# Kernel optimization log

Hardware: AMD Instinct MI355X
Metric: run time of the kernel (lower is better)

## Reference

```python
import jax, jax.numpy as jnp
import numpy as np

WINDOW_SIZE = 20
NEG_BIG = -1e8  # matches -10**8 in the torch mask


def band_mask(S):
    # 0 inside the sliding window |i-j| <= WINDOW_SIZE, -1e8 outside (additive mask)
    idx = jnp.arange(S)
    return jnp.where(jnp.abs(idx[:, None] - idx[None, :]) <= WINDOW_SIZE, 0.0, NEG_BIG).astype(jnp.float32)


def setup_inputs() -> dict:
    key = jax.random.key(0)
    k1, k2, k3, k4 = jax.random.split(key, 4)
    B, S, Dq, Dk = 8, 2048, 1024, 1024
    queries = jax.random.normal(k1, (B, S, Dq), dtype=jnp.float32)
    keys = jax.random.normal(k2, (B, S, Dk), dtype=jnp.float32)
    # reduce = nn.Linear(key_dim, query_dim) since key_dim >= query_dim
    lim = 1.0 / np.sqrt(Dk)
    W_reduce = jax.random.uniform(k3, (Dq, Dk), jnp.float32, -lim, lim)
    b_reduce = jax.random.uniform(k4, (Dq,), jnp.float32, -lim, lim)
    return {"queries": queries, "keys": keys, "W_reduce": W_reduce, "b_reduce": b_reduce}


def reference(queries, keys, W_reduce, b_reduce):
    # values default to the ORIGINAL keys (before dim matching)
    values = keys
    # match_dims: reduce keys to query_dim
    keys_r = jnp.einsum('bkd,qd->bkq', keys, W_reduce) + b_reduce  # [B,S,Dq]
    sims = jnp.einsum('bqd,bkd->bqk', queries, keys_r)             # [B,S,S]
    sims = sims + band_mask(queries.shape[1])                      # additive banded window mask
    weights = jax.nn.softmax(sims, axis=-1)
    return jnp.einsum('bqk,bkd->bqd', weights, values)
```

## Files before the change

kernel.cpp:

```cpp
#include <hip/hip_runtime.h>


#define BATCH 8
#define SEQ   2048
#define DIM   1024
#define WIN   20

typedef _Float16 half8  __attribute__((ext_vector_type(8)));
typedef _Float16 half4v __attribute__((ext_vector_type(4)));
typedef float    f32x4  __attribute__((ext_vector_type(4)));

#define GLOAD_LDS16(gsrc, ldst)                                                        \
    __builtin_amdgcn_global_load_lds(                                                  \
        (const __attribute__((address_space(1))) void*)(gsrc),                         \
        (__attribute__((address_space(3))) void*)(ldst), 16, 0, 0)

__global__ __launch_bounds__(256) void cvt_q_f16(const float* __restrict__ in,
                                                 _Float16* __restrict__ out) {
    const int n8 = (BATCH * SEQ * DIM) / 8;
    for (int i = blockIdx.x * 256 + threadIdx.x; i < n8; i += gridDim.x * 256) {
        const float4 a = ((const float4*)in)[2 * i];
        const float4 b = ((const float4*)in)[2 * i + 1];
        half8 h;
        h[0] = (_Float16)a.x; h[1] = (_Float16)a.y; h[2] = (_Float16)a.z; h[3] = (_Float16)a.w;
        h[4] = (_Float16)b.x; h[5] = (_Float16)b.y; h[6] = (_Float16)b.z; h[7] = (_Float16)b.w;
        ((half8*)out)[i] = h;
    }
}

#define WTS 68
__global__ __launch_bounds__(256) void cvt_w_t(const float* __restrict__ W,
                                               _Float16* __restrict__ WT) {
    __shared__ _Float16 tile[64 * WTS];
    const int k0 = blockIdx.x * 64;
    const int n0 = blockIdx.y * 64;
    const int t  = threadIdx.x;
    const int r  = t >> 4;
    const int c4 = (t & 15) * 4;
    #pragma unroll
    for (int rr = 0; rr < 64; rr += 16) {
        float4 v = *(const float4*)&W[(size_t)(k0 + rr + r) * DIM + n0 + c4];
        _Float16* dst = &tile[(rr + r) * WTS + c4];
        dst[0] = (_Float16)v.x; dst[1] = (_Float16)v.y;
        dst[2] = (_Float16)v.z; dst[3] = (_Float16)v.w;
    }
    __syncthreads();
    #pragma unroll
    for (int rr = 0; rr < 64; rr += 16) {
        const int n = rr + r;
        half4v h = { tile[(c4 + 0) * WTS + n], tile[(c4 + 1) * WTS + n],
                     tile[(c4 + 2) * WTS + n], tile[(c4 + 3) * WTS + n] };
        *(half4v*)&WT[(size_t)(n0 + n) * DIM + k0 + c4] = h;
    }
}

#define GK 64
__global__ __launch_bounds__(256, 2) void gemm_f16t(const _Float16* __restrict__ A,
                                                    const _Float16* __restrict__ B,
                                                    _Float16* __restrict__ C) {
    __shared__ _Float16 As[128 * GK];
    __shared__ _Float16 Bs[128 * GK];

    const int m0   = blockIdx.y * 128;
    const int n0   = blockIdx.x * 128;
    const int t    = threadIdx.x;
    const int lane = t & 63;
    const int wv   = t >> 6;
    const int wm   = (wv >> 1) * 64;
    const int wn   = (wv & 1) * 64;
    const int l15  = lane & 15;
    const int quad = lane >> 4;

    const int srow = lane >> 3;
    const int sck  = (lane & 7) ^ srow;

    f32x4 acc[4][4] = {};

    for (int k0 = 0; k0 < DIM; k0 += GK) {
        __syncthreads();
        #pragma unroll
        for (int j = 0; j < 4; ++j) {
            const int rs = (j * 4 + wv) * 8;
            GLOAD_LDS16(A + (size_t)(m0 + rs + srow) * DIM + k0 + sck * 8, &As[rs * GK]);
            GLOAD_LDS16(B + (size_t)(n0 + rs + srow) * DIM + k0 + sck * 8, &Bs[rs * GK]);
        }
        __syncthreads();

        #pragma unroll
        for (int s = 0; s < 2; ++s) {
            half8 af[4], bf[4];
            #pragma unroll
            for (int i = 0; i < 4; ++i)
                af[i] = *(const half8*)&As[(wm + i * 16 + l15) * GK +
                                           (((s * 4 + quad) ^ (l15 & 7)) * 8)];
            #pragma unroll
            for (int j = 0; j < 4; ++j)
                bf[j] = *(const half8*)&Bs[(wn + j * 16 + l15) * GK +
                                           (((s * 4 + quad) ^ (l15 & 7)) * 8)];
            #pragma unroll
            for (int i = 0; i < 4; ++i)
                #pragma unroll
                for (int j = 0; j < 4; ++j)
                    acc[i][j] = __builtin_amdgcn_mfma_f32_16x16x32_f16(af[i], bf[j], acc[i][j], 0, 0, 0);
        }
    }

    #pragma unroll
    for (int i = 0; i < 4; ++i) {
        #pragma unroll
        for (int r = 0; r < 4; ++r) {
            _Float16* crow = C + (size_t)(m0 + wm + i * 16 + quad * 4 + r) * DIM + n0 + wn + l15;
            #pragma unroll
            for (int j = 0; j < 4; ++j)
                crow[j * 16] = (_Float16)acc[i][j][r];
        }
    }
}

#define TQV  32
#define KSR  96
#define KLD2 80
#define QLD2 80
#define SLD2 84
#define PLD  104

__global__ __launch_bounds__(512, 4) void attn_v5(const _Float16* __restrict__ QT,
                                                  const float* __restrict__ Keys,
                                                  float* __restrict__ Out) {
    const int blk  = blockIdx.x;
    const int b    = blk & 7;
    const int tile = blk >> 3;
    const int q0   = tile * TQV;
    const int t    = threadIdx.x;
    const int lane = t & 63;
    const int wv   = t >> 6;
    const int l15  = lane & 15;
    const int quad = lane >> 4;

    const int klo = (q0 - WIN) > 0 ? (q0 - WIN) : 0;
    const int khi = (q0 + TQV - 1 + WIN) < (SEQ - 1) ? (q0 + TQV - 1 + WIN) : (SEQ - 1);
    const int nk  = khi - klo + 1;

    const float* keys = Keys + (size_t)b * SEQ * DIM;

    __shared__ _Float16 Qc[TQV * QLD2];
    __shared__ _Float16 Ks[KSR * KLD2];
    __shared__ float    Sl[TQV * SLD2];
    __shared__ _Float16 Pl[TQV * PLD];

    const int qr = t >> 4;
    const int qc = (t & 15) * 4;
    const int kr = t >> 3;
    const int kc = (t & 7) * 8;
    const int krow0 = (klo + kr) < (SEQ - 1) ? (klo + kr) : (SEQ - 1);
    const int kr2   = 64 + (t >> 3);
    const int krow2 = (klo + kr2) < (SEQ - 1) ? (klo + kr2) : (SEQ - 1);

    const _Float16* qsrc  = QT + ((size_t)b * SEQ + q0 + qr) * DIM + qc;
    const float*    ksrc0 = keys + (size_t)krow0 * DIM + kc;
    const float*    ksrc2 = keys + (size_t)krow2 * DIM + kc;

    const int qt_w = wv >> 2;
    const int kt_a = wv & 3;
    const bool two = (kt_a == 0);

    f32x4 acc0 = {}, acc1 = {};

    for (int d0 = 0; d0 < DIM; d0 += 64) {
        half4v hq = *(const half4v*)(qsrc + d0);
        float4 kv0 = *(const float4*)(ksrc0 + d0);
        float4 kv1 = *(const float4*)(ksrc0 + d0 + 4);
        float4 kv2, kv3;
        if (t < 128) {
            kv2 = *(const float4*)(ksrc2 + d0);
            kv3 = *(const float4*)(ksrc2 + d0 + 4);
        }

        __syncthreads();

        *(half4v*)&Qc[qr * QLD2 + qc] = hq;
        half8 h0;
        h0[0] = (_Float16)kv0.x; h0[1] = (_Float16)kv0.y;
        h0[2] = (_Float16)kv0.z; h0[3] = (_Float16)kv0.w;
        h0[4] = (_Float16)kv1.x; h0[5] = (_Float16)kv1.y;
        h0[6] = (_Float16)kv1.z; h0[7] = (_Float16)kv1.w;
        *(half8*)&Ks[kr * KLD2 + kc] = h0;
        if (t < 128) {
            half8 h2;
            h2[0] = (_Float16)kv2.x; h2[1] = (_Float16)kv2.y;
            h2[2] = (_Float16)kv2.z; h2[3] = (_Float16)kv2.w;
            h2[4] = (_Float16)kv3.x; h2[5] = (_Float16)kv3.y;
            h2[6] = (_Float16)kv3.z; h2[7] = (_Float16)kv3.w;
            *(half8*)&Ks[kr2 * KLD2 + kc] = h2;
        }

        __syncthreads();

        #pragma unroll
        for (int s = 0; s < 2; ++s) {
            half8 af = *(const half8*)&Qc[(qt_w * 16 + l15) * QLD2 + s * 32 + quad * 8];
            half8 bf0 = *(const half8*)&Ks[(kt_a * 16 + l15) * KLD2 + s * 32 + quad * 8];
            acc0 = __builtin_amdgcn_mfma_f32_16x16x32_f16(af, bf0, acc0, 0, 0, 0);
            if (two) {
                half8 bf1 = *(const half8*)&Ks[(4 * 16 + l15) * KLD2 + s * 32 + quad * 8];
                acc1 = __builtin_amdgcn_mfma_f32_16x16x32_f16(af, bf1, acc1, 0, 0, 0);
            }
        }
    }

    __syncthreads();
    #pragma unroll
    for (int r = 0; r < 4; ++r) {
        const int q = qt_w * 16 + quad * 4 + r;
        {
            const int c = kt_a * 16 + l15;
            const int d = (q0 + q) - (klo + c);
            const bool valid = (c < nk) && ((unsigned)(d + WIN) <= 2u * WIN);
            Sl[q * SLD2 + c] = valid ? acc0[r] : -1e30f;
        }
        if (two) {
            const int c = 64 + l15;
            const int d = (q0 + q) - (klo + c);
            const bool valid = (c < nk) && ((unsigned)(d + WIN) <= 2u * WIN);
            Sl[q * SLD2 + c] = valid ? acc1[r] : -1e30f;
        }
    }
    __syncthreads();

    if (t < 128) {
        const int q = t >> 2, part = t & 3;
        const float* srow = &Sl[q * SLD2 + part * 20];
        _Float16*    prow = &Pl[q * PLD + part * 20];
        float m = -1e30f;
        float e[20];
        #pragma unroll
        for (int i = 0; i < 20; ++i) m = fmaxf(m, srow[i]);
        m = fmaxf(m, __shfl_xor(m, 1));
        m = fmaxf(m, __shfl_xor(m, 2));
        float ssum = 0.f;
        #pragma unroll
        for (int i = 0; i < 20; ++i) { e[i] = expf(srow[i] - m); ssum += e[i]; }
        ssum += __shfl_xor(ssum, 1);
        ssum += __shfl_xor(ssum, 2);
        const float inv = 1.f / ssum;
        #pragma unroll
        for (int i = 0; i < 20; ++i) prow[i] = (_Float16)(e[i] * inv);
        if (part == 3) {
            #pragma unroll
            for (int i = 0; i < 16; ++i) Pl[q * PLD + 80 + i] = (_Float16)0.f;
        }
    }
    __syncthreads();

    const int dt_w = wv & 3;
    const int kr2b  = 64 + (t >> 3);
    const int krow2b = (klo + kr2b) < (SEQ - 1) ? (klo + kr2b) : (SEQ - 1);
    const float* ksrc2b = keys + (size_t)krow2b * DIM + kc;

    for (int ch = 0; ch < 16; ++ch) {
        const int d0 = ch * 64;
        float4 kv0 = *(const float4*)(ksrc0 + d0);
        float4 kv1 = *(const float4*)(ksrc0 + d0 + 4);
        float4 kv2, kv3;
        if (t < 256) {
            kv2 = *(const float4*)(ksrc2b + d0);
            kv3 = *(const float4*)(ksrc2b + d0 + 4);
        }

        __syncthreads();

        half8 h0;
        h0[0] = (_Float16)kv0.x; h0[1] = (_Float16)kv0.y;
        h0[2] = (_Float16)kv0.z; h0[3] = (_Float16)kv0.w;
        h0[4] = (_Float16)kv1.x; h0[5] = (_Float16)kv1.y;
        h0[6] = (_Float16)kv1.z; h0[7] = (_Float16)kv1.w;
        *(half8*)&Ks[kr * KLD2 + kc] = h0;
        if (t < 256) {
            half8 h2;
            h2[0] = (_Float16)kv2.x; h2[1] = (_Float16)kv2.y;
            h2[2] = (_Float16)kv2.z; h2[3] = (_Float16)kv2.w;
            h2[4] = (_Float16)kv3.x; h2[5] = (_Float16)kv3.y;
            h2[6] = (_Float16)kv3.z; h2[7] = (_Float16)kv3.w;
            *(half8*)&Ks[kr2b * KLD2 + kc] = h2;
        }

        __syncthreads();

        f32x4 accO = {};
        #pragma unroll
        for (int s = 0; s < 3; ++s) {
            half8 af = *(const half8*)&Pl[(qt_w * 16 + l15) * PLD + s * 32 + quad * 8];
            half8 bf;
            #pragma unroll
            for (int j = 0; j < 8; ++j)
                bf[j] = Ks[(s * 32 + quad * 8 + j) * KLD2 + dt_w * 16 + l15];
            accO = __builtin_amdgcn_mfma_f32_16x16x32_f16(af, bf, accO, 0, 0, 0);
        }
        #pragma unroll
        for (int r = 0; r < 4; ++r)
            Out[((size_t)b * SEQ + q0 + qt_w * 16 + quad * 4 + r) * DIM + d0 + dt_w * 16 + l15] = accO[r];
    }
}

#define LDK 40
__global__ __launch_bounds__(256) void gemm_qw_f16(const float* __restrict__ Q,
                                                   const float* __restrict__ W,
                                                   float* __restrict__ QT) {
    __shared__ _Float16 Asl[128 * LDK];
    __shared__ _Float16 Bsl[128 * LDK];

    const int m0 = blockIdx.x * 128;
    const int n0 = blockIdx.y * 128;
    const int t  = threadIdx.x;
    const int lane = t & 63;
    const int wv   = t >> 6;
    const int wm   = (wv >> 1) * 64;
    const int wn   = (wv & 1) * 64;
    const int l15  = lane & 15;
    const int quad = lane >> 4;

    const int ar = t >> 1;
    const int ac = (t & 1) * 16;
    const float* Aptr = Q + (size_t)(m0 + ar) * DIM + ac;
    _Float16* AsW = &Asl[ar * LDK + ac];

    const int br = t >> 3;
    const int bc = t & 7;
    const float* Bptr = W + (size_t)br * DIM + n0 + bc;

    f32x4 acc[4][4] = {};

    for (int k0 = 0; k0 < DIM; k0 += 32) {
        float4 a0 = *(const float4*)(Aptr + k0);
        float4 a1 = *(const float4*)(Aptr + k0 + 4);
        float4 a2 = *(const float4*)(Aptr + k0 + 8);
        float4 a3 = *(const float4*)(Aptr + k0 + 12);
        float bv[16];
        #pragma unroll
        for (int j = 0; j < 16; ++j) bv[j] = Bptr[(size_t)k0 * DIM + 8 * j];

        __syncthreads();

        half8 h0, h1;
        h0[0] = (_Float16)a0.x; h0[1] = (_Float16)a0.y; h0[2] = (_Float16)a0.z; h0[3] = (_Float16)a0.w;
        h0[4] = (_Float16)a1.x; h0[5] = (_Float16)a1.y; h0[6] = (_Float16)a1.z; h0[7] = (_Float16)a1.w;
        h1[0] = (_Float16)a2.x; h1[1] = (_Float16)a2.y; h1[2] = (_Float16)a2.z; h1[3] = (_Float16)a2.w;
        h1[4] = (_Float16)a3.x; h1[5] = (_Float16)a3.y; h1[6] = (_Float16)a3.z; h1[7] = (_Float16)a3.w;
        *(half8*)(AsW)     = h0;
        *(half8*)(AsW + 8) = h1;

        #pragma unroll
        for (int j = 0; j < 16; ++j)
            Bsl[(bc + 8 * j) * LDK + br] = (_Float16)bv[j];

        __syncthreads();

        half8 af[4], bf[4];
        #pragma unroll
        for (int i = 0; i < 4; ++i)
            af[i] = *(const half8*)&Asl[(wm + i * 16 + l15) * LDK + quad * 8];
        #pragma unroll
        for (int j = 0; j < 4; ++j)
            bf[j] = *(const half8*)&Bsl[(wn + j * 16 + l15) * LDK + quad * 8];

        #pragma unroll
        for (int i = 0; i < 4; ++i)
            #pragma unroll
            for (int j = 0; j < 4; ++j)
                acc[i][j] = __builtin_amdgcn_mfma_f32_16x16x32_f16(af[i], bf[j], acc[i][j], 0, 0, 0);
    }

    #pragma unroll
    for (int i = 0; i < 4; ++i) {
        const int row0 = m0 + wm + i * 16 + quad * 4;
        #pragma unroll
        for (int r = 0; r < 4; ++r) {
            float* orow = QT + (size_t)(row0 + r) * DIM + n0 + wn + l15;
            #pragma unroll
            for (int j = 0; j < 4; ++j)
                orow[j * 16] = acc[i][j][r];
        }
    }
}

#define TQ  16
#define KP  64
#define KLD 80
#define QLD 80
#define SLD 66

__global__ __launch_bounds__(256, 4) void attn_fb(const float* __restrict__ QT,
                                                  const float* __restrict__ Keys,
                                                  float* __restrict__ Out) {
    const int blk  = blockIdx.x;
    const int b    = blk & 7;
    const int tile = blk >> 3;
    const int q0   = tile * TQ;
    const int t    = threadIdx.x;
    const int lane = t & 63;
    const int wv   = t >> 6;
    const int l15  = lane & 15;
    const int quad = lane >> 4;

    const int klo = (q0 - WIN) > 0 ? (q0 - WIN) : 0;
    const int khi = (q0 + TQ - 1 + WIN) < (SEQ - 1) ? (q0 + TQ - 1 + WIN) : (SEQ - 1);
    const int nk  = khi - klo + 1;

    const float* qt   = QT + ((size_t)b * SEQ + q0) * DIM;
    const float* keys = Keys + (size_t)b * SEQ * DIM;

    __shared__ _Float16 Qc[TQ * QLD];
    __shared__ _Float16 Ks[KP * KLD];
    __shared__ float    Sl[TQ * SLD];
    __shared__ float    Wl[TQ * SLD];

    const int qr = t >> 4;
    const int qc = (t & 15) * 4;
    const int kr = t >> 2;
    const int kc = (t & 3) * 4;
    const int krow = (klo + kr) < (SEQ - 1) ? (klo + kr) : (SEQ - 1);

    const float* qsrc = qt + (size_t)qr * DIM + qc;
    const float* ksrc = keys + (size_t)krow * DIM + kc;

    f32x4 acc_s = {};

    for (int d0 = 0; d0 < DIM; d0 += 64) {
        const float4 qv = *(const float4*)(qsrc + d0);
        float4 kv0 = *(const float4*)(ksrc + d0);
        float4 kv1 = *(const float4*)(ksrc + d0 + 16);
        float4 kv2 = *(const float4*)(ksrc + d0 + 32);
        float4 kv3 = *(const float4*)(ksrc + d0 + 48);

        __syncthreads();

        half4v hq = {(_Float16)qv.x, (_Float16)qv.y, (_Float16)qv.z, (_Float16)qv.w};
        *(half4v*)&Qc[qr * QLD + qc] = hq;
        half4v h0 = {(_Float16)kv0.x, (_Float16)kv0.y, (_Float16)kv0.z, (_Float16)kv0.w};
        half4v h1 = {(_Float16)kv1.x, (_Float16)kv1.y, (_Float16)kv1.z, (_Float16)kv1.w};
        half4v h2 = {(_Float16)kv2.x, (_Float16)kv2.y, (_Float16)kv2.z, (_Float16)kv2.w};
        half4v h3 = {(_Float16)kv3.x, (_Float16)kv3.y, (_Float16)kv3.z, (_Float16)kv3.w};
        *(half4v*)&Ks[kr * KLD + kc]      = h0;
        *(half4v*)&Ks[kr * KLD + kc + 16] = h1;
        *(half4v*)&Ks[kr * KLD + kc + 32] = h2;
        *(half4v*)&Ks[kr * KLD + kc + 48] = h3;

        __syncthreads();

        #pragma unroll
        for (int s = 0; s < 2; ++s) {
            half8 af = *(const half8*)&Qc[l15 * QLD + s * 32 + quad * 8];
            half8 bf = *(const half8*)&Ks[(wv * 16 + l15) * KLD + s * 32 + quad * 8];
            acc_s = __builtin_amdgcn_mfma_f32_16x16x32_f16(af, bf, acc_s, 0, 0, 0);
        }
    }

    __syncthreads();
    #pragma unroll
    for (int r = 0; r < 4; ++r) {
        const int q = quad * 4 + r;
        const int c = wv * 16 + l15;
        const int d = (q0 + q) - (klo + c);
        const bool valid = (c < nk) && ((unsigned)(d + WIN) <= 2u * WIN);
        Sl[q * SLD + c] = valid ? acc_s[r] : -1e30f;
    }
    __syncthreads();

    if (t < 64) {
        const int q = t >> 2, part = t & 3;
        const float* srow = &Sl[q * SLD + part * 16];
        float*       wrow = &Wl[q * SLD + part * 16];
        float m = -1e30f;
        #pragma unroll
        for (int i = 0; i < 16; ++i) m = fmaxf(m, srow[i]);
        m = fmaxf(m, __shfl_xor(m, 1));
        m = fmaxf(m, __shfl_xor(m, 2));
        float ssum = 0.f;
        #pragma unroll
        for (int i = 0; i < 16; ++i) { float e = expf(srow[i] - m); wrow[i] = e; ssum += e; }
        ssum += __shfl_xor(ssum, 1);
        ssum += __shfl_xor(ssum, 2);
        const float inv = 1.f / ssum;
        #pragma unroll
        for (int i = 0; i < 16; ++i) wrow[i] *= inv;
    }
    __syncthreads();

    float accs[TQ][4] = {};
    for (int c = 0; c < nk; ++c) {
        const float* krow2 = keys + (size_t)(klo + c) * DIM;
        const float k0 = krow2[t], k1 = krow2[t + 256], k2 = krow2[t + 512], k3 = krow2[t + 768];
        #pragma unroll
        for (int q = 0; q < TQ; ++q) {
            const float w = Wl[q * SLD + c];
            accs[q][0] = fmaf(w, k0, accs[q][0]);
            accs[q][1] = fmaf(w, k1, accs[q][1]);
            accs[q][2] = fmaf(w, k2, accs[q][2]);
            accs[q][3] = fmaf(w, k3, accs[q][3]);
        }
    }
    #pragma unroll
    for (int q = 0; q < TQ; ++q) {
        float* orow = Out + ((size_t)b * SEQ + q0 + q) * DIM;
        orow[t]       = accs[q][0];
        orow[t + 256] = accs[q][1];
        orow[t + 512] = accs[q][2];
        orow[t + 768] = accs[q][3];
    }
}

extern "C" void kernel_launch(void* const* d_in, const int* in_sizes, int n_in,
                              void* d_out, int out_size, void* d_ws, size_t ws_size,
                              hipStream_t stream) {
    const float* queries = (const float*)d_in[0];
    const float* keys    = (const float*)d_in[1];
    const float* W       = (const float*)d_in[2];
    float* out = (float*)d_out;

    const size_t qt16_bytes = (size_t)BATCH * SEQ * DIM * sizeof(_Float16);
    const size_t w16_bytes  = (size_t)DIM * DIM * sizeof(_Float16);

    if (ws_size >= qt16_bytes + w16_bytes) {
        _Float16* q16  = (_Float16*)d_out;
        _Float16* qt16 = (_Float16*)d_ws;
        _Float16* w16t = (_Float16*)((char*)d_ws + qt16_bytes);

        cvt_q_f16<<<2048, 256, 0, stream>>>(queries, q16);
        cvt_w_t<<<dim3(16, 16), 256, 0, stream>>>(W, w16t);
        gemm_f16t<<<dim3(8, 128), 256, 0, stream>>>(q16, w16t, qt16);
        const int nblk = (BATCH * SEQ) / TQV;
        attn_v5<<<nblk, 512, 0, stream>>>(qt16, keys, out);
    } else {
        gemm_qw_f16<<<dim3(128, 8), 256, 0, stream>>>(queries, W, out);
        const int nblk = (BATCH * SEQ) / TQ;
        attn_fb<<<nblk, 256, 0, stream>>>(out, keys, out);
    }
}
```

Baseline: 251.2 us.

## Read value keys directly from global memory in PV stage and swizzle GEMM block order

The PV stage of the attention kernel no longer stages fp32 key chunks into shared memory with two barriers per chunk. Each lane now loads its B-fragment elements directly from global memory (strided by row) and converts them to fp16, so the per-chunk syncthreads go away and the key shared buffer shrinks. The Q·W GEMM switches to a 1D grid with a swizzled block-to-tile mapping to improve L2 locality. The direct loads are scalar, row-strided 4-byte reads, which may coalesce poorly and raise memory traffic, though each row segment is 64 bytes contiguous across l15 lanes.

```diff
diff --git a/kernel.cpp b/kernel.cpp
--- a/kernel.cpp
+++ b/kernel.cpp
@@ -61,8 +61,9 @@
     __shared__ _Float16 As[128 * GK];
     __shared__ _Float16 Bs[128 * GK];
 
-    const int m0   = blockIdx.y * 128;
-    const int n0   = blockIdx.x * 128;
+    const int bid  = blockIdx.x;
+    const int m0   = (((bid & 7) << 4) | (bid >> 6)) * 128;
+    const int n0   = ((bid >> 3) & 7) * 128;
     const int t    = threadIdx.x;
     const int lane = t & 63;
     const int wv   = t >> 6;
@@ -118,13 +119,13 @@
 }
 
 #define TQV  32
-#define KSR  96
+#define KSR  80
 #define KLD2 80
 #define QLD2 80
 #define SLD2 84
 #define PLD  104
 
-__global__ __launch_bounds__(512, 4) void attn_v5(const _Float16* __restrict__ QT,
+__global__ __launch_bounds__(512, 4) void attn_v6(const _Float16* __restrict__ QT,
                                                   const float* __restrict__ Keys,
                                                   float* __restrict__ Out) {
     const int blk  = blockIdx.x;
@@ -253,52 +254,25 @@
     __syncthreads();
 
     const int dt_w = wv & 3;
-    const int kr2b  = 64 + (t >> 3);
-    const int krow2b = (klo + kr2b) < (SEQ - 1) ? (klo + kr2b) : (SEQ - 1);
-    const float* ksrc2b = keys + (size_t)krow2b * DIM + kc;
-
     for (int ch = 0; ch < 16; ++ch) {
-        const int d0 = ch * 64;
-        float4 kv0 = *(const float4*)(ksrc0 + d0);
-        float4 kv1 = *(const float4*)(ksrc0 + d0 + 4);
-        float4 kv2, kv3;
-        if (t < 256) {
-            kv2 = *(const float4*)(ksrc2b + d0);
-            kv3 = *(const float4*)(ksrc2b + d0 + 4);
-        }
-
-        __syncthreads();
-
-        half8 h0;
-        h0[0] = (_Float16)kv0.x; h0[1] = (_Float16)kv0.y;
-        h0[2] = (_Float16)kv0.z; h0[3] = (_Float16)kv0.w;
-        h0[4] = (_Float16)kv1.x; h0[5] = (_Float16)kv1.y;
-        h0[6] = (_Float16)kv1.z; h0[7] = (_Float16)kv1.w;
-        *(half8*)&Ks[kr * KLD2 + kc] = h0;
-        if (t < 256) {
-            half8 h2;
-            h2[0] = (_Float16)kv2.x; h2[1] = (_Float16)kv2.y;
-            h2[2] = (_Float16)kv2.z; h2[3] = (_Float16)kv2.w;
-            h2[4] = (_Float16)kv3.x; h2[5] = (_Float16)kv3.y;
-            h2[6] = (_Float16)kv3.z; h2[7] = (_Float16)kv3.w;
-            *(half8*)&Ks[kr2b * KLD2 + kc] = h2;
-        }
-
-        __syncthreads();
-
+        const int dcol = ch * 64 + dt_w * 16 + l15;
+        const float* kcol = keys + dcol;
         f32x4 accO = {};
         #pragma unroll
         for (int s = 0; s < 3; ++s) {
             half8 af = *(const half8*)&Pl[(qt_w * 16 + l15) * PLD + s * 32 + quad * 8];
             half8 bf;
             #pragma unroll
-            for (int j = 0; j < 8; ++j)
-                bf[j] = Ks[(s * 32 + quad * 8 + j) * KLD2 + dt_w * 16 + l15];
+            for (int j = 0; j < 8; ++j) {
+                int c = s * 32 + quad * 8 + j;
+                int kr3 = klo + c; if (kr3 > SEQ - 1) kr3 = SEQ - 1;
+                bf[j] = (_Float16)kcol[(size_t)kr3 * DIM];
+            }
             accO = __builtin_amdgcn_mfma_f32_16x16x32_f16(af, bf, accO, 0, 0, 0);
         }
         #pragma unroll
         for (int r = 0; r < 4; ++r)
-            Out[((size_t)b * SEQ + q0 + qt_w * 16 + quad * 4 + r) * DIM + d0 + dt_w * 16 + l15] = accO[r];
+            Out[((size_t)b * SEQ + q0 + qt_w * 16 + quad * 4 + r) * DIM + dcol] = accO[r];
     }
 }
 
@@ -527,9 +501,9 @@
 
         cvt_q_f16<<<2048, 256, 0, stream>>>(queries, q16);
         cvt_w_t<<<dim3(16, 16), 256, 0, stream>>>(W, w16t);
-        gemm_f16t<<<dim3(8, 128), 256, 0, stream>>>(q16, w16t, qt16);
+        gemm_f16t<<<1024, 256, 0, stream>>>(q16, w16t, qt16);
         const int nblk = (BATCH * SEQ) / TQV;
-        attn_v5<<<nblk, 512, 0, stream>>>(qt16, keys, out);
+        attn_v6<<<nblk, 512, 0, stream>>>(qt16, keys, out);
     } else {
         gemm_qw_f16<<<dim3(128, 8), 256, 0, stream>>>(queries, W, out);
         const int nblk = (BATCH * SEQ) / TQ;
```

Measured after the change: 249.6 us. About the same (-0.6%).
